# Kernel tuning notes

Hardware: AMD Instinct MI355X
Metric: run time of the kernel (lower is better)

## Reference

```python
import jax, jax.numpy as jnp
import numpy as np

B, H, W = 4, 64, 64
INPLANES, PLANES, G, K = 608, 152, 19, 3
KK = K * K
EPS = 1e-5


def conv2d(x, w, stride=1, padding=0, dilation=1):
    return jax.lax.conv_general_dilated(
        x, w, (stride, stride), [(padding, padding)] * 2,
        rhs_dilation=(dilation, dilation),
        dimension_numbers=("NCHW", "OIHW", "NCHW"))


def bn(x, g, b, m, v):
    # inference-mode batchnorm (affine with running stats)
    inv = g / jnp.sqrt(v + EPS)
    return x * inv[None, :, None, None] + (b - m * inv)[None, :, None, None]


def deform_conv(x, offset, w, pad=1, dil=1):
    # x: [B,C,H,W], offset: [B, 2*G*KK, H, W] ((dy,dx) pairs per group per tap), w: [Cout,C,K,K]
    Bs, C, Hh, Ww = x.shape
    Cg = C // G
    off = offset.reshape(Bs, G, KK, 2, Hh, Ww)
    ky, kx = jnp.meshgrid(jnp.arange(K), jnp.arange(K), indexing="ij")
    base_y = (jnp.arange(Hh) - pad)[None, None, None, :, None] + (dil * ky.reshape(-1))[None, None, :, None, None]
    base_x = (jnp.arange(Ww) - pad)[None, None, None, None, :] + (dil * kx.reshape(-1))[None, None, :, None, None]
    ys = base_y + off[:, :, :, 0]  # [B,G,KK,H,W]
    xs = base_x + off[:, :, :, 1]
    y0 = jnp.floor(ys)
    x0 = jnp.floor(xs)
    wy = ys - y0
    wx = xs - x0
    y0i = y0.astype(jnp.int32)
    x0i = x0.astype(jnp.int32)
    xf = x.reshape(Bs, G, Cg, Hh * Ww)

    def gather(yi, xi, wgt):
        valid = ((yi >= 0) & (yi < Hh) & (xi >= 0) & (xi < Ww)).astype(x.dtype)
        idx = jnp.clip(yi, 0, Hh - 1) * Ww + jnp.clip(xi, 0, Ww - 1)
        idxf = jnp.broadcast_to(idx.reshape(Bs, G, 1, KK * Hh * Ww), (Bs, G, Cg, KK * Hh * Ww))
        g = jnp.take_along_axis(xf, idxf, axis=3).reshape(Bs, G, Cg, KK, Hh, Ww)
        return g * (wgt * valid)[:, :, None]

    samp = (gather(y0i, x0i, (1 - wy) * (1 - wx))
            + gather(y0i, x0i + 1, (1 - wy) * wx)
            + gather(y0i + 1, x0i, wy * (1 - wx))
            + gather(y0i + 1, x0i + 1, wy * wx))  # [B,G,Cg,KK,H,W]
    wr = w.reshape(w.shape[0], G, Cg, KK)
    return jnp.einsum("bgckhw,ogck->bohw", samp, wr)


def setup_inputs() -> dict:
    key = jax.random.key(0)
    ks = jax.random.split(key, 8)
    d = {}
    d["x"] = jax.random.normal(ks[0], (B, INPLANES, H, W), jnp.float32)
    d["conv1_w"] = jax.random.normal(ks[1], (PLANES, INPLANES, 1, 1), jnp.float32) * 0.05
    d["conv2_w"] = jax.random.normal(ks[2], (2 * G * KK, PLANES, 3, 3), jnp.float32) * 0.01
    d["dconv_w"] = jax.random.normal(ks[3], (PLANES, PLANES, 3, 3), jnp.float32) * 0.05
    d["conv3_w"] = jax.random.normal(ks[4], (4 * PLANES, PLANES, 1, 1), jnp.float32) * 0.05
    for i, (name, c) in enumerate([("bn1", PLANES), ("bn2", PLANES), ("bn3", 4 * PLANES)]):
        k1, k2, k3, k4 = jax.random.split(ks[5 + i], 4)
        d[name + "_g"] = jax.random.uniform(k1, (c,), jnp.float32, 0.5, 1.5)
        d[name + "_b"] = jax.random.normal(k2, (c,), jnp.float32) * 0.1
        d[name + "_m"] = jax.random.normal(k3, (c,), jnp.float32) * 0.1
        d[name + "_v"] = jax.random.uniform(k4, (c,), jnp.float32, 0.5, 1.5)
    return d


def reference(x, conv1_w, conv2_w, dconv_w, conv3_w,
              bn1_g, bn1_b, bn1_m, bn1_v,
              bn2_g, bn2_b, bn2_m, bn2_v,
              bn3_g, bn3_b, bn3_m, bn3_v):
    out = jax.nn.relu(conv2d(x, conv1_w))           # conv1 -> relu (order as in source)
    out = bn(out, bn1_g, bn1_b, bn1_m, bn1_v)       # -> bn1
    offset = conv2d(out, conv2_w, padding=1)         # offset-generating 3x3 conv
    out = deform_conv(out, offset, dconv_w)          # deformable 3x3 conv
    out = bn(jax.nn.relu(out), bn2_g, bn2_b, bn2_m, bn2_v)
    out = bn(conv2d(out, conv3_w), bn3_g, bn3_b, bn3_m, bn3_v)
    return jax.nn.relu(out + x)
```

## Files before the change

### kernel.cpp

```cpp
#include <hip/hip_runtime.h>

#define EPSV 1e-5f

typedef __bf16 bf16_t;
typedef __bf16 bf16x8 __attribute__((ext_vector_type(8)));
typedef float f32x4 __attribute__((ext_vector_type(4)));

__device__ inline bf16x8 bzero8() {
  bf16x8 z;
#pragma unroll
  for (int i = 0; i < 8; i++) z[i] = (bf16_t)0.f;
  return z;
}

__device__ inline f32x4 mfma16(bf16x8 a, bf16x8 b, f32x4 c) {
  return __builtin_amdgcn_mfma_f32_16x16x32_bf16(a, b, c, 0, 0, 0);
}

#define W1E (160 * 608)
#define W2E (384 * 1376)
#define WDE (192 * 1440)
#define W3E (640 * 160)

__global__ __launch_bounds__(256) void prep_weights(
    const float* __restrict__ w1, const float* __restrict__ w2,
    const float* __restrict__ wd, const float* __restrict__ w3,
    bf16_t* __restrict__ w1b, bf16_t* __restrict__ w2b,
    bf16_t* __restrict__ wdb, bf16_t* __restrict__ w3b) {
  int i = blockIdx.x * 256 + threadIdx.x;
  float v = 0.f;
  if (i < W1E) {
    int oc = i / 608, ic = i % 608;
    if (oc < 152) v = w1[oc * 608 + ic];
    w1b[i] = (bf16_t)v;
  } else if (i < W1E + W2E) {
    int j = i - W1E;
    int oc = j / 1376, k = j % 1376;
    if (oc < 342 && k < 1368) {
      int t = k / 152, ic = k % 152;
      v = w2[(oc * 152 + ic) * 9 + t];
    }
    w2b[j] = (bf16_t)v;
  } else if (i < W1E + W2E + WDE) {
    int j = i - W1E - W2E;
    int o = j / 1440, k = j % 1440;
    int t = k / 160, ic = k % 160;
    if (o < 152 && ic < 152) v = wd[(o * 152 + ic) * 9 + t];
    wdb[j] = (bf16_t)v;
  } else if (i < W1E + W2E + WDE + W3E) {
    int j = i - W1E - W2E - WDE;
    int oc = j / 160, ic = j % 160;
    if (oc < 608 && ic < 152) v = w3[oc * 152 + ic];
    w3b[j] = (bf16_t)v;
  }
}

__global__ void prep_bn(const float* g1, const float* b1, const float* m1, const float* v1,
                        const float* g2, const float* b2, const float* m2, const float* v2,
                        const float* g3, const float* b3, const float* m3, const float* v3,
                        float* __restrict__ bnc) {
  int i = threadIdx.x;
  if (i < 152) {
    float inv = g1[i] / sqrtf(v1[i] + EPSV);
    bnc[i] = inv;
    bnc[152 + i] = b1[i] - m1[i] * inv;
    float inv2 = g2[i] / sqrtf(v2[i] + EPSV);
    bnc[304 + i] = inv2;
    bnc[456 + i] = b2[i] - m2[i] * inv2;
  }
  if (i < 608) {
    float inv3 = g3[i] / sqrtf(v3[i] + EPSV);
    bnc[608 + i] = inv3;
    bnc[1216 + i] = b3[i] - m3[i] * inv3;
  }
}

__global__ __launch_bounds__(256) void s1_conv1(const float* __restrict__ x,
                                                const bf16_t* __restrict__ w1b,
                                                const float* __restrict__ bnc,
                                                bf16_t* __restrict__ out1) {
  __shared__ bf16_t t1[32 * 616];
  int tid = threadIdx.x;
  int px0 = blockIdx.x * 32;
  int b = px0 >> 12, sp0 = px0 & 4095;
  for (int task = tid; task < 608 * 8; task += 256) {
    int c = task >> 3, i4 = task & 7;
    f32x4 v = *(const f32x4*)(x + (((size_t)(b * 608 + c)) << 12) + sp0 + i4 * 4);
#pragma unroll
    for (int i = 0; i < 4; i++) t1[(i4 * 4 + i) * 616 + c] = (bf16_t)v[i];
  }
  __syncthreads();
  int wid = tid >> 6, lane = tid & 63, q = lane >> 4, lr = lane & 15;
  int mw = wid & 1, nw = wid >> 1;
  f32x4 acc[5];
#pragma unroll
  for (int n = 0; n < 5; n++) acc[n] = (f32x4){0.f, 0.f, 0.f, 0.f};
  for (int kk = 0; kk < 19; kk++) {
    int k0 = kk * 32 + q * 8;
    bf16x8 a = *(const bf16x8*)(t1 + (mw * 16 + lr) * 616 + k0);
#pragma unroll
    for (int n = 0; n < 5; n++) {
      bf16x8 bf = *(const bf16x8*)(w1b + (nw * 80 + n * 16 + lr) * 608 + k0);
      acc[n] = mfma16(a, bf, acc[n]);
    }
  }
#pragma unroll
  for (int n = 0; n < 5; n++) {
    int oc = nw * 80 + n * 16 + lr;
    if (oc < 152) {
      float inv = bnc[oc], beta = bnc[152 + oc];
#pragma unroll
      for (int i = 0; i < 4; i++) {
        int p = px0 + mw * 16 + q * 4 + i;
        float v = fmaxf(acc[n][i], 0.f) * inv + beta;
        out1[(size_t)p * 152 + oc] = (bf16_t)v;
      }
    }
  }
}

__global__ __launch_bounds__(512) void s2_offs(const bf16_t* __restrict__ out1,
                                               const bf16_t* __restrict__ w2b,
                                               float* __restrict__ offs) {
  __shared__ bf16_t t2[102 * 152];
  int tid = threadIdx.x;
  int xh = blockIdx.x & 1, y = (blockIdx.x >> 1) & 63, b = blockIdx.x >> 7;
  const bf16_t* ob = out1 + (((size_t)b) << 12) * 152;
  int x0 = xh * 32 - 1;
  for (int task = tid; task < 3 * 34 * 19; task += 512) {
    int j = task / 646, r = task % 646;
    int xi = r / 19, cb = r % 19;
    int yy = y + j - 1, xx = x0 + xi;
    bf16x8 v = bzero8();
    if (yy >= 0 && yy < 64 && xx >= 0 && xx < 64)
      v = *(const bf16x8*)(ob + (size_t)(yy * 64 + xx) * 152 + cb * 8);
    *(bf16x8*)(t2 + (j * 34 + xi) * 152 + cb * 8) = v;
  }
  __syncthreads();
  int wid = tid >> 6, lane = tid & 63, q = lane >> 4, lr = lane & 15;
  f32x4 acc[2][3];
#pragma unroll
  for (int m = 0; m < 2; m++)
#pragma unroll
    for (int n = 0; n < 3; n++) acc[m][n] = (f32x4){0.f, 0.f, 0.f, 0.f};
  for (int kk = 0; kk < 43; kk++) {
    int k0 = kk * 32 + q * 8;
    bf16x8 a[2];
    if (k0 < 1368) {
      int t = k0 / 152, c0 = k0 - t * 152;
      int dy = t / 3, dxp1 = t - dy * 3;
      int base = (dy * 34 + lr + dxp1) * 152 + c0;
#pragma unroll
      for (int m = 0; m < 2; m++) a[m] = *(const bf16x8*)(t2 + base + m * 16 * 152);
    } else {
      a[0] = bzero8();
      a[1] = bzero8();
    }
#pragma unroll
    for (int n = 0; n < 3; n++) {
      bf16x8 bf = *(const bf16x8*)(w2b + (size_t)(wid * 48 + n * 16 + lr) * 1376 + k0);
#pragma unroll
      for (int m = 0; m < 2; m++) acc[m][n] = mfma16(a[m], bf, acc[m][n]);
    }
  }
#pragma unroll
  for (int n = 0; n < 3; n++) {
    int col = wid * 48 + n * 16 + lr;
    if (col < 342) {
      int g = col / 18, rem = col % 18;
      int t = rem >> 1, c = rem & 1;
      int pos = t * 38 + g * 2 + c;
#pragma unroll
      for (int m = 0; m < 2; m++)
#pragma unroll
        for (int i = 0; i < 4; i++) {
          int p = (b << 12) + y * 64 + xh * 32 + m * 16 + q * 4 + i;
          offs[(size_t)p * 344 + pos] = acc[m][n][i];
        }
    }
  }
}

__global__ __launch_bounds__(256, 4) void s3_dconv(const bf16_t* __restrict__ out1,
                                                   const float* __restrict__ offs,
                                                   const bf16_t* __restrict__ wdb,
                                                   const float* __restrict__ bnc,
                                                   bf16_t* __restrict__ a2) {
  __shared__ float olds[16 * 344];
  __shared__ bf16_t abuf[2 * 16 * 168];
  int tid = threadIdx.x;
  int row0 = blockIdx.x * 16;
  int bb = row0 >> 12;
  const bf16_t* obase = out1 + (((size_t)bb << 12) * 152);
  if (tid < 64) {
    int cur = tid >> 5, r = (tid >> 1) & 15, ch = tid & 1;
    *(bf16x8*)(abuf + cur * 2688 + r * 168 + 152 + ch * 8) = bzero8();
  }
  for (int task = tid; task < 16 * 86; task += 256) {
    int r = task / 86, cc = task - r * 86;
    *(f32x4*)(olds + r * 344 + cc * 4) =
        *(const f32x4*)(offs + (size_t)(row0 + r) * 344 + cc * 4);
  }
  __syncthreads();

  int wid = tid >> 6, lane = tid & 63, q = lane >> 4, lr = lane & 15;
  f32x4 acc[3];
#pragma unroll
  for (int n = 0; n < 3; n++) acc[n] = (f32x4){0.f, 0.f, 0.f, 0.f};

#define SAMPLE_TAP(T, CUR)                                                        \
  {                                                                               \
    int t_ = (T);                                                                 \
    int ky = t_ / 3, kx = t_ - ky * 3;                                            \
    for (int task = tid; task < 304; task += 256) {                               \
      int r = task / 19, g = task - r * 19;                                       \
      int p = row0 + r;                                                           \
      int y = (p >> 6) & 63, xc = p & 63;                                         \
      float2 ov = *(const float2*)(olds + r * 344 + t_ * 38 + g * 2);             \
      float ys = (float)(y - 1 + ky) + ov.x;                                      \
      float xs = (float)(xc - 1 + kx) + ov.y;                                     \
      float y0f = floorf(ys), x0f = floorf(xs);                                   \
      float wy = ys - y0f, wx = xs - x0f;                                         \
      int y0 = (int)y0f, x0 = (int)x0f;                                           \
      int y1 = y0 + 1, x1 = x0 + 1;                                               \
      int y0c = min(max(y0, 0), 63), x0c = min(max(x0, 0), 63);                   \
      int y1c = min(max(y1, 0), 63), x1c = min(max(x1, 0), 63);                   \
      float vy0 = (y0 == y0c) ? 1.f : 0.f;                                        \
      float vy1 = (y1 == y1c) ? 1.f : 0.f;                                        \
      float vx0 = (x0 == x0c) ? 1.f : 0.f;                                        \
      float vx1 = (x1 == x1c) ? 1.f : 0.f;                                        \
      float w00 = (1.f - wy) * (1.f - wx) * vy0 * vx0;                            \
      float w01 = (1.f - wy) * wx * vy0 * vx1;                                    \
      float w10 = wy * (1.f - wx) * vy1 * vx0;                                    \
      float w11 = wy * wx * vy1 * vx1;                                            \
      const bf16_t* bg = obase + g * 8;                                           \
      bf16x8 c00 = *(const bf16x8*)(bg + (size_t)(y0c * 64 + x0c) * 152);         \
      bf16x8 c01 = *(const bf16x8*)(bg + (size_t)(y0c * 64 + x1c) * 152);         \
      bf16x8 c10 = *(const bf16x8*)(bg + (size_t)(y1c * 64 + x0c) * 152);         \
      bf16x8 c11 = *(const bf16x8*)(bg + (size_t)(y1c * 64 + x1c) * 152);         \
      bf16x8 o;                                                                   \
      _Pragma("unroll") for (int i = 0; i < 8; i++) {                             \
        float f = w00 * (float)c00[i];                                            \
        f = fmaf(w01, (float)c01[i], f);                                          \
        f = fmaf(w10, (float)c10[i], f);                                          \
        f = fmaf(w11, (float)c11[i], f);                                          \
        o[i] = (bf16_t)f;                                                         \
      }                                                                           \
      *(bf16x8*)(abuf + (CUR)*2688 + r * 168 + g * 8) = o;                        \
    }                                                                             \
  }

  SAMPLE_TAP(0, 0)
  __syncthreads();
  for (int t = 0; t < 9; t++) {
    int cur = t & 1;
    if (t < 8) SAMPLE_TAP(t + 1, cur ^ 1)
#pragma unroll
    for (int kk = 0; kk < 5; kk++) {
      int k0 = kk * 32 + q * 8;
      bf16x8 a = *(const bf16x8*)(abuf + cur * 2688 + lr * 168 + k0);
#pragma unroll
      for (int n = 0; n < 3; n++) {
        bf16x8 bf = *(const bf16x8*)(wdb + (size_t)((wid * 3 + n) * 16 + lr) * 1440 + t * 160 + k0);
        acc[n] = mfma16(a, bf, acc[n]);
      }
    }
    __syncthreads();
  }
#pragma unroll
  for (int n = 0; n < 3; n++) {
    int oc = (wid * 3 + n) * 16 + lr;
    if (oc < 152) {
      float inv = bnc[304 + oc], beta = bnc[456 + oc];
#pragma unroll
      for (int i = 0; i < 4; i++) {
        int p = row0 + q * 4 + i;
        float v = fmaxf(acc[n][i], 0.f) * inv + beta;
        a2[(size_t)p * 152 + oc] = (bf16_t)v;
      }
    }
  }
#undef SAMPLE_TAP
}

__global__ __launch_bounds__(256) void s4_conv3(const bf16_t* __restrict__ a2,
                                                const bf16_t* __restrict__ w3b,
                                                const float* __restrict__ bnc,
                                                const float* __restrict__ x,
                                                float* __restrict__ out) {
  int tid = threadIdx.x;
  int wid = tid >> 6, lane = tid & 63, q = lane >> 4, lr = lane & 15;
  int p0 = blockIdx.x * 16;
  int b = p0 >> 12, sp0 = p0 & 4095;
  f32x4 acc[10];
#pragma unroll
  for (int n = 0; n < 10; n++) acc[n] = (f32x4){0.f, 0.f, 0.f, 0.f};
  for (int kk = 0; kk < 5; kk++) {
    int k0 = kk * 32 + q * 8;
    bf16x8 a = (k0 < 152) ? *(const bf16x8*)(a2 + (size_t)(p0 + lr) * 152 + k0) : bzero8();
#pragma unroll
    for (int n = 0; n < 10; n++) {
      bf16x8 bf = *(const bf16x8*)(w3b + (size_t)(wid * 160 + n * 16 + lr) * 160 + k0);
      acc[n] = mfma16(a, bf, acc[n]);
    }
  }
#pragma unroll
  for (int n = 0; n < 10; n++) {
    int oc = wid * 160 + n * 16 + lr;
    if (oc < 608) {
      float inv = bnc[608 + oc], beta = bnc[1216 + oc];
      size_t gi = (((size_t)(b * 608 + oc)) << 12) + sp0 + q * 4;
      f32x4 xr = *(const f32x4*)(x + gi);
      f32x4 o;
#pragma unroll
      for (int i = 0; i < 4; i++) o[i] = fmaxf(acc[n][i] * inv + beta + xr[i], 0.f);
      *(f32x4*)(out + gi) = o;
    }
  }
}

extern "C" void kernel_launch(void* const* d_in, const int* in_sizes, int n_in,
                              void* d_out, int out_size, void* d_ws, size_t ws_size,
                              hipStream_t stream) {
  const float* x = (const float*)d_in[0];
  const float* w1 = (const float*)d_in[1];
  const float* w2 = (const float*)d_in[2];
  const float* wd = (const float*)d_in[3];
  const float* w3 = (const float*)d_in[4];
  const float* g1 = (const float*)d_in[5];
  const float* b1 = (const float*)d_in[6];
  const float* m1 = (const float*)d_in[7];
  const float* v1 = (const float*)d_in[8];
  const float* g2 = (const float*)d_in[9];
  const float* b2 = (const float*)d_in[10];
  const float* m2 = (const float*)d_in[11];
  const float* v2 = (const float*)d_in[12];
  const float* g3 = (const float*)d_in[13];
  const float* b3 = (const float*)d_in[14];
  const float* m3 = (const float*)d_in[15];
  const float* v3 = (const float*)d_in[16];

  char* ws = (char*)d_ws;
  bf16_t* w1b = (bf16_t*)(ws + 0);
  bf16_t* w2b = (bf16_t*)(ws + 194560);
  bf16_t* wdb = (bf16_t*)(ws + 1251328);
  bf16_t* w3b = (bf16_t*)(ws + 1804288);
  float* bnc = (float*)(ws + 2009088);
  bf16_t* out1 = (bf16_t*)(ws + 2016384);
  float* offs = (float*)(ws + 6997120);
  bf16_t* a2 = (bf16_t*)(ws + 29541504);
  float* out = (float*)d_out;

  prep_weights<<<3924, 256, 0, stream>>>(w1, w2, wd, w3, w1b, w2b, wdb, w3b);
  prep_bn<<<1, 640, 0, stream>>>(g1, b1, m1, v1, g2, b2, m2, v2, g3, b3, m3, v3, bnc);
  s1_conv1<<<512, 256, 0, stream>>>(x, w1b, bnc, out1);
  s2_offs<<<512, 512, 0, stream>>>(out1, w2b, offs);
  s3_dconv<<<1024, 256, 0, stream>>>(out1, offs, wdb, bnc, a2);
  s4_conv3<<<1024, 256, 0, stream>>>(a2, w3b, bnc, x, out);
}
```

Before: 176.7 us.

## Restructure offset conv: wider per-wave N tile, register-prefetched weights, padded LDS

```diff
diff --git a/kernel.cpp b/kernel.cpp
--- a/kernel.cpp
+++ b/kernel.cpp
@@ -119,63 +119,72 @@
   }
 }
 
-__global__ __launch_bounds__(512) void s2_offs(const bf16_t* __restrict__ out1,
-                                               const bf16_t* __restrict__ w2b,
-                                               float* __restrict__ offs) {
-  __shared__ bf16_t t2[102 * 152];
+__global__ __launch_bounds__(256, 5) void s2_offs(const bf16_t* __restrict__ out1,
+                                                  const bf16_t* __restrict__ w2b,
+                                                  float* __restrict__ offs) {
+  __shared__ bf16_t t2[3 * 34 * 156];
   int tid = threadIdx.x;
   int xh = blockIdx.x & 1, y = (blockIdx.x >> 1) & 63, b = blockIdx.x >> 7;
   const bf16_t* ob = out1 + (((size_t)b) << 12) * 152;
   int x0 = xh * 32 - 1;
-  for (int task = tid; task < 3 * 34 * 19; task += 512) {
+  for (int task = tid; task < 3 * 34 * 19; task += 256) {
     int j = task / 646, r = task % 646;
     int xi = r / 19, cb = r % 19;
     int yy = y + j - 1, xx = x0 + xi;
     bf16x8 v = bzero8();
     if (yy >= 0 && yy < 64 && xx >= 0 && xx < 64)
       v = *(const bf16x8*)(ob + (size_t)(yy * 64 + xx) * 152 + cb * 8);
-    *(bf16x8*)(t2 + (j * 34 + xi) * 152 + cb * 8) = v;
+    *(bf16x8*)(t2 + (j * 34 + xi) * 156 + cb * 8) = v;
   }
   __syncthreads();
   int wid = tid >> 6, lane = tid & 63, q = lane >> 4, lr = lane & 15;
-  f32x4 acc[2][3];
+  f32x4 acc[2][6];
 #pragma unroll
   for (int m = 0; m < 2; m++)
 #pragma unroll
-    for (int n = 0; n < 3; n++) acc[m][n] = (f32x4){0.f, 0.f, 0.f, 0.f};
+    for (int n = 0; n < 6; n++) acc[m][n] = (f32x4){0.f, 0.f, 0.f, 0.f};
+  const bf16_t* wb = w2b + (size_t)lr * 1376;
+  bf16x8 bcur[6];
+#pragma unroll
+  for (int n = 0; n < 6; n++)
+    bcur[n] = *(const bf16x8*)(wb + (size_t)(wid * 96 + n * 16) * 1376 + q * 8);
   for (int kk = 0; kk < 43; kk++) {
     int k0 = kk * 32 + q * 8;
+    bf16x8 bnx[6];
+    if (kk < 42) {
+      int k1 = k0 + 32;
+#pragma unroll
+      for (int n = 0; n < 6; n++)
+        bnx[n] = *(const bf16x8*)(wb + (size_t)(wid * 96 + n * 16) * 1376 + k1);
+    }
     bf16x8 a[2];
     if (k0 < 1368) {
       int t = k0 / 152, c0 = k0 - t * 152;
       int dy = t / 3, dxp1 = t - dy * 3;
-      int base = (dy * 34 + lr + dxp1) * 152 + c0;
-#pragma unroll
-      for (int m = 0; m < 2; m++) a[m] = *(const bf16x8*)(t2 + base + m * 16 * 152);
+#pragma unroll
+      for (int m = 0; m < 2; m++)
+        a[m] = *(const bf16x8*)(t2 + (dy * 34 + m * 16 + lr + dxp1) * 156 + c0);
     } else {
       a[0] = bzero8();
       a[1] = bzero8();
     }
 #pragma unroll
-    for (int n = 0; n < 3; n++) {
-      bf16x8 bf = *(const bf16x8*)(w2b + (size_t)(wid * 48 + n * 16 + lr) * 1376 + k0);
-#pragma unroll
-      for (int m = 0; m < 2; m++) acc[m][n] = mfma16(a[m], bf, acc[m][n]);
-    }
-  }
-#pragma unroll
-  for (int n = 0; n < 3; n++) {
-    int col = wid * 48 + n * 16 + lr;
+    for (int n = 0; n < 6; n++)
+#pragma unroll
+      for (int m = 0; m < 2; m++) acc[m][n] = mfma16(a[m], bcur[n], acc[m][n]);
+#pragma unroll
+    for (int n = 0; n < 6; n++) bcur[n] = bnx[n];
+  }
+#pragma unroll
+  for (int n = 0; n < 6; n++) {
+    int col = wid * 96 + n * 16 + lr;
     if (col < 342) {
-      int g = col / 18, rem = col % 18;
-      int t = rem >> 1, c = rem & 1;
-      int pos = t * 38 + g * 2 + c;
 #pragma unroll
       for (int m = 0; m < 2; m++)
 #pragma unroll
         for (int i = 0; i < 4; i++) {
           int p = (b << 12) + y * 64 + xh * 32 + m * 16 + q * 4 + i;
-          offs[(size_t)p * 344 + pos] = acc[m][n][i];
+          offs[(size_t)p * 344 + col] = acc[m][n][i];
         }
     }
   }
@@ -216,7 +225,7 @@
       int r = task / 19, g = task - r * 19;                                       \
       int p = row0 + r;                                                           \
       int y = (p >> 6) & 63, xc = p & 63;                                         \
-      float2 ov = *(const float2*)(olds + r * 344 + t_ * 38 + g * 2);             \
+      float2 ov = *(const float2*)(olds + r * 344 + g * 18 + t_ * 2);             \
       float ys = (float)(y - 1 + ky) + ov.x;                                      \
       float xs = (float)(xc - 1 + kx) + ov.y;                                     \
       float y0f = floorf(ys), x0f = floorf(xs);                                   \
@@ -354,7 +363,7 @@
   prep_weights<<<3924, 256, 0, stream>>>(w1, w2, wd, w3, w1b, w2b, wdb, w3b);
   prep_bn<<<1, 640, 0, stream>>>(g1, b1, m1, v1, g2, b2, m2, v2, g3, b3, m3, v3, bnc);
   s1_conv1<<<512, 256, 0, stream>>>(x, w1b, bnc, out1);
-  s2_offs<<<512, 512, 0, stream>>>(out1, w2b, offs);
+  s2_offs<<<512, 256, 0, stream>>>(out1, w2b, offs);
   s3_dconv<<<1024, 256, 0, stream>>>(out1, offs, wdb, bnc, a2);
   s4_conv3<<<1024, 256, 0, stream>>>(a2, w3b, bnc, x, out);
 }
```

New measurement: 173.9 us. About the same (-1.6%).
